# Kernel tuning notes

Measured on AMD Instinct MI355X. Metric: run time of the kernel, lower is better.

The kernel has to match this reference:

```python
import jax, jax.numpy as jnp
import numpy as np


def _lstm(x, w_ih, w_hh, b_ih, b_hh):
    # x: [B, T, D]; w_ih: [4H, D]; w_hh: [4H, H]. PyTorch gate order: i, f, g, o.
    B, T, D = x.shape
    H = w_hh.shape[1]
    # Precompute input contributions for all timesteps: [B, T, 4H]
    xg = jnp.einsum('btd,gd->btg', x, w_ih) + b_ih + b_hh
    xg = jnp.transpose(xg, (1, 0, 2))  # [T, B, 4H]

    def step(carry, xt):
        h, c = carry
        gates = xt + h @ w_hh.T  # [B, 4H]
        i, f, g, o = jnp.split(gates, 4, axis=-1)
        i = jax.nn.sigmoid(i)
        f = jax.nn.sigmoid(f)
        g = jnp.tanh(g)
        o = jax.nn.sigmoid(o)
        c = f * c + i * g
        h = o * jnp.tanh(c)
        return (h, c), h

    h0 = jnp.zeros((B, H), dtype=x.dtype)
    c0 = jnp.zeros((B, H), dtype=x.dtype)
    (_, _), hs = jax.lax.scan(step, (h0, c0), xg)
    return jnp.transpose(hs, (1, 0, 2))  # [B, T, H]


def setup_inputs() -> dict:
    key = jax.random.key(0)
    ks = jax.random.split(key, 11)
    B, T, D, H1, H2, OUT = 2048, 128, 128, 128, 64, 64
    s1 = 1.0 / np.sqrt(H1)
    s2 = 1.0 / np.sqrt(H2)
    return {
        'x': jax.random.normal(ks[0], (B, T, D), dtype=jnp.float32),
        'w_ih1': jax.random.uniform(ks[1], (4 * H1, D), jnp.float32, -s1, s1),
        'w_hh1': jax.random.uniform(ks[2], (4 * H1, H1), jnp.float32, -s1, s1),
        'b_ih1': jax.random.uniform(ks[3], (4 * H1,), jnp.float32, -s1, s1),
        'b_hh1': jax.random.uniform(ks[4], (4 * H1,), jnp.float32, -s1, s1),
        'w_ih2': jax.random.uniform(ks[5], (4 * H2, H1), jnp.float32, -s2, s2),
        'w_hh2': jax.random.uniform(ks[6], (4 * H2, H2), jnp.float32, -s2, s2),
        'b_ih2': jax.random.uniform(ks[7], (4 * H2,), jnp.float32, -s2, s2),
        'b_hh2': jax.random.uniform(ks[8], (4 * H2,), jnp.float32, -s2, s2),
        'w_dense': jax.random.uniform(ks[9], (OUT, H2), jnp.float32, -s2, s2),
        'b_dense': jax.random.uniform(ks[10], (OUT,), jnp.float32, -s2, s2),
    }


def reference(x, w_ih1, w_hh1, b_ih1, b_hh1, w_ih2, w_hh2, b_ih2, b_hh2, w_dense, b_dense):
    # Dropout is identity in eval mode.
    h = _lstm(x, w_ih1, w_hh1, b_ih1, b_hh1)          # [B, T, H1]
    h = _lstm(h, w_ih2, w_hh2, b_ih2, b_hh2)          # [B, T, H2]
    last = h[:, -1, :]                                 # [B, H2]
    return jax.nn.relu(last @ w_dense.T + b_dense)     # [B, 64]
```

## Files before the change

### kernel.cpp

```cpp
#include <hip/hip_runtime.h>
#include <hip/hip_bf16.h>

#define BB  2048
#define TT  128
#define DD  128
#define HH1 128
#define GG1 512
#define HH2 64
#define GG2 256
#define OO  64

typedef __attribute__((ext_vector_type(8))) short  short8;
typedef __attribute__((ext_vector_type(4))) float  floatx4;

#define PIN(x) asm volatile("" : "+v"(x))

#define OFF_WHH1 0
#define OFF_WIH1 131072
#define OFF_WIH2 262144
#define OFF_WHH2 327680
#define OFF_B1   360448
#define OFF_B2   362496
#define OFF_XBF  524288
#define OFF_H1S  67633152

__device__ __forceinline__ short f2bf(float f) {
  unsigned u = __float_as_uint(f);
  unsigned r = (u + 0x7FFFu + ((u >> 16) & 1u)) >> 16;
  return (short)r;
}
__device__ __forceinline__ float sigm(float x) {
  return __builtin_amdgcn_rcpf(1.0f + __expf(-x));
}
__device__ __forceinline__ float tanh_fast(float x) {
  return 1.0f - 2.0f * __builtin_amdgcn_rcpf(1.0f + __expf(2.0f * x));
}

__global__ void k_prep(const float* __restrict__ wih1, const float* __restrict__ whh1,
                       const float* __restrict__ bih1, const float* __restrict__ bhh1,
                       const float* __restrict__ wih2, const float* __restrict__ whh2,
                       const float* __restrict__ bih2, const float* __restrict__ bhh2,
                       char* __restrict__ ws) {
  short* WHH1 = (short*)(ws + OFF_WHH1);
  short* WIH1 = (short*)(ws + OFF_WIH1);
  short* WIH2 = (short*)(ws + OFF_WIH2);
  short* WHH2 = (short*)(ws + OFF_WHH2);
  float* B1 = (float*)(ws + OFF_B1);
  float* B2 = (float*)(ws + OFF_B2);
  int idx = blockIdx.x * blockDim.x + threadIdx.x;
  int stride = gridDim.x * blockDim.x;
  for (int i = idx; i < GG1 * DD; i += stride) { WIH1[i] = f2bf(wih1[i]); WHH1[i] = f2bf(whh1[i]); }
  for (int i = idx; i < GG2 * HH1; i += stride) WIH2[i] = f2bf(wih2[i]);
  for (int i = idx; i < GG2 * HH2; i += stride) WHH2[i] = f2bf(whh2[i]);
  for (int i = idx; i < GG1; i += stride) B1[i] = bih1[i] + bhh1[i];
  for (int i = idx; i < GG2; i += stride) B2[i] = bih2[i] + bhh2[i];
}

__global__ __launch_bounds__(256) void k_xcast(const float* __restrict__ x,
                                               short* __restrict__ xbf) {
  size_t i = ((size_t)blockIdx.x * 256 + threadIdx.x) * 8;
  float4 a = *(const float4*)&x[i];
  float4 b = *(const float4*)&x[i + 4];
  short8 o;
  o[0] = f2bf(a.x); o[1] = f2bf(a.y); o[2] = f2bf(a.z); o[3] = f2bf(a.w);
  o[4] = f2bf(b.x); o[5] = f2bf(b.y); o[6] = f2bf(b.z); o[7] = f2bf(b.w);
  *(short8*)&xbf[i] = o;
}

__global__ __launch_bounds__(512, 2) void k_rec1f(const char* __restrict__ ws,
                                                  short* __restrict__ h1s) {
  __shared__ short hbds[2][16 * 136];
  const short* WHH = (const short*)(ws + OFF_WHH1);
  const short* WIH = (const short*)(ws + OFF_WIH1);
  const short* XBF = (const short*)(ws + OFF_XBF);
  const float* B1 = (const float*)(ws + OFF_B1);
  const int lane = threadIdx.x & 63;
  const int wv = threadIdx.x >> 6;
  const int col = lane & 15, quad = lane >> 4;
  const int hc = wv * 16 + col;
  const int r0 = blockIdx.x * 8;

  short8 wh[4][4], wx[4][4];
#pragma unroll
  for (int gt = 0; gt < 4; ++gt)
#pragma unroll
    for (int kk = 0; kk < 4; ++kk) {
      wh[gt][kk] = *(const short8*)&WHH[(gt * 128 + hc) * HH1 + kk * 32 + quad * 8];
      wx[gt][kk] = *(const short8*)&WIH[(gt * 128 + hc) * DD + kk * 32 + quad * 8];
      PIN(wh[gt][kk]);
      PIN(wx[gt][kk]);
    }
  float bias[4];
#pragma unroll
  for (int gt = 0; gt < 4; ++gt) bias[gt] = B1[gt * 128 + hc];

  for (int i = threadIdx.x; i < 2 * 16 * 136; i += 512) ((short*)hbds)[i] = 0;

  const bool aload = (col < 8);
  const short* xbase = XBF + (size_t)(r0 + (col & 7)) * TT * DD;
  short8 ax_cur[4], ax_nxt[4];
#pragma unroll
  for (int kk = 0; kk < 4; ++kk) {
    short8 z = {0, 0, 0, 0, 0, 0, 0, 0};
    ax_cur[kk] = aload ? *(const short8*)&xbase[kk * 32 + quad * 8] : z;
    ax_nxt[kk] = z;
  }

  const int row0 = (quad & 1) * 4 + (quad >> 1) * 2;
  float c0 = 0.f, c1 = 0.f;
  __syncthreads();

  auto step = [&](int t, short* rbuf, short* wbuf) {
    if (t + 1 < TT && aload) {
#pragma unroll
      for (int kk = 0; kk < 4; ++kk)
        ax_nxt[kk] = *(const short8*)&xbase[(t + 1) * DD + kk * 32 + quad * 8];
    }
    floatx4 acc[4];
#pragma unroll
    for (int gt = 0; gt < 4; ++gt)
      acc[gt] = (floatx4){bias[gt], bias[gt], bias[gt], bias[gt]};
#pragma unroll
    for (int kk = 0; kk < 4; ++kk)
#pragma unroll
      for (int gt = 0; gt < 4; ++gt)
        acc[gt] = __builtin_amdgcn_mfma_f32_16x16x32_bf16(ax_cur[kk], wx[gt][kk], acc[gt], 0, 0, 0);
    short8 ah[4];
#pragma unroll
    for (int kk = 0; kk < 4; ++kk)
      ah[kk] = *(const short8*)&rbuf[col * 136 + kk * 32 + quad * 8];
#pragma unroll
    for (int kk = 0; kk < 4; ++kk)
#pragma unroll
      for (int gt = 0; gt < 4; ++gt)
        acc[gt] = __builtin_amdgcn_mfma_f32_16x16x32_bf16(ah[kk], wh[gt][kk], acc[gt], 0, 0, 0);

    float g0[4], g1[4];
#pragma unroll
    for (int gt = 0; gt < 4; ++gt) {
      float v2 = __shfl_xor(acc[gt][2], 32);
      float v3 = __shfl_xor(acc[gt][3], 32);
      g0[gt] = (quad < 2) ? acc[gt][0] : v2;
      g1[gt] = (quad < 2) ? acc[gt][1] : v3;
    }
    {
      float i0 = sigm(g0[0]), f0 = sigm(g0[1]), gg0 = tanh_fast(g0[2]), o0 = sigm(g0[3]);
      c0 = fmaf(f0, c0, i0 * gg0);
      float hA = o0 * tanh_fast(c0);
      float i1 = sigm(g1[0]), f1 = sigm(g1[1]), gg1 = tanh_fast(g1[2]), o1 = sigm(g1[3]);
      c1 = fmaf(f1, c1, i1 * gg1);
      float hB = o1 * tanh_fast(c1);
      short ha = f2bf(hA), hbv = f2bf(hB);
      wbuf[(row0)     * 136 + hc] = ha;
      wbuf[(row0 + 1) * 136 + hc] = hbv;
      h1s[((size_t)(r0 + row0)     * TT + t) * HH1 + hc] = ha;
      h1s[((size_t)(r0 + row0 + 1) * TT + t) * HH1 + hc] = hbv;
    }
    __syncthreads();
#pragma unroll
    for (int kk = 0; kk < 4; ++kk) ax_cur[kk] = ax_nxt[kk];
  };

  for (int t = 0; t < TT; t += 2) {
    step(t,     &hbds[0][0], &hbds[1][0]);
    step(t + 1, &hbds[1][0], &hbds[0][0]);
  }
}

__global__ __launch_bounds__(512, 2) void k_rec2f(const char* __restrict__ ws,
                                                  const short* __restrict__ h1s,
                                                  const float* __restrict__ wd,
                                                  const float* __restrict__ bd,
                                                  float* __restrict__ out) {
  __shared__ short hbuf[16 * 72];
  __shared__ float gsm[8 * 260];
  __shared__ float h2f[8 * HH2];
  const short* WHH = (const short*)(ws + OFF_WHH2);
  const short* WIH = (const short*)(ws + OFF_WIH2);
  const float* B2 = (const float*)(ws + OFF_B2);
  const int lane = threadIdx.x & 63;
  const int wv = threadIdx.x >> 6;
  const int col = lane & 15, quad = lane >> 4;
  const int n0 = wv * 32;
  const int r0 = blockIdx.x * 8;

  short8 wh[2][2], wx[2][4];
#pragma unroll
  for (int nt = 0; nt < 2; ++nt) {
#pragma unroll
    for (int kk = 0; kk < 2; ++kk) {
      wh[nt][kk] = *(const short8*)&WHH[(n0 + nt * 16 + col) * HH2 + kk * 32 + quad * 8];
      PIN(wh[nt][kk]);
    }
#pragma unroll
    for (int kk = 0; kk < 4; ++kk) {
      wx[nt][kk] = *(const short8*)&WIH[(n0 + nt * 16 + col) * HH1 + kk * 32 + quad * 8];
      PIN(wx[nt][kk]);
    }
  }
  float bias[2];
#pragma unroll
  for (int nt = 0; nt < 2; ++nt) bias[nt] = B2[n0 + nt * 16 + col];

  for (int i = threadIdx.x; i < 16 * 72; i += 512) hbuf[i] = 0;

  const bool aload = (col < 8);
  const short* h1base = h1s + (size_t)(r0 + (col & 7)) * TT * HH1;
  short8 ax_cur[4], ax_nxt[4];
#pragma unroll
  for (int kk = 0; kk < 4; ++kk) {
    short8 z = {0, 0, 0, 0, 0, 0, 0, 0};
    ax_cur[kk] = aload ? *(const short8*)&h1base[kk * 32 + quad * 8] : z;
    ax_nxt[kk] = z;
  }

  const int j = threadIdx.x & 63;
  const int rr = threadIdx.x >> 6;
  float cc = 0.f;
  __syncthreads();

  for (int t = 0; t < TT; ++t) {
    if (t + 1 < TT && aload) {
#pragma unroll
      for (int kk = 0; kk < 4; ++kk)
        ax_nxt[kk] = *(const short8*)&h1base[(t + 1) * HH1 + kk * 32 + quad * 8];
    }
    floatx4 acc[2];
#pragma unroll
    for (int nt = 0; nt < 2; ++nt)
      acc[nt] = (floatx4){bias[nt], bias[nt], bias[nt], bias[nt]};
#pragma unroll
    for (int kk = 0; kk < 4; ++kk)
#pragma unroll
      for (int nt = 0; nt < 2; ++nt)
        acc[nt] = __builtin_amdgcn_mfma_f32_16x16x32_bf16(ax_cur[kk], wx[nt][kk], acc[nt], 0, 0, 0);
    short8 ah[2];
#pragma unroll
    for (int kk = 0; kk < 2; ++kk)
      ah[kk] = *(const short8*)&hbuf[col * 72 + kk * 32 + quad * 8];
#pragma unroll
    for (int kk = 0; kk < 2; ++kk)
#pragma unroll
      for (int nt = 0; nt < 2; ++nt)
        acc[nt] = __builtin_amdgcn_mfma_f32_16x16x32_bf16(ah[kk], wh[nt][kk], acc[nt], 0, 0, 0);

    if (quad < 2) {
#pragma unroll
      for (int nt = 0; nt < 2; ++nt)
#pragma unroll
        for (int r = 0; r < 4; ++r)
          gsm[(quad * 4 + r) * 260 + n0 + nt * 16 + col] = acc[nt][r];
    }
    __syncthreads();

    {
      float i0 = gsm[rr * 260 + j],       f0 = gsm[rr * 260 + 64 + j];
      float g0 = gsm[rr * 260 + 128 + j], o0 = gsm[rr * 260 + 192 + j];
      cc = fmaf(sigm(f0), cc, sigm(i0) * tanh_fast(g0));
      float hh = sigm(o0) * tanh_fast(cc);
      hbuf[rr * 72 + j] = f2bf(hh);
      if (t == TT - 1) h2f[rr * HH2 + j] = hh;
    }
    __syncthreads();
#pragma unroll
    for (int kk = 0; kk < 4; ++kk) ax_cur[kk] = ax_nxt[kk];
  }

  {
    const int o = threadIdx.x & 63;
    const int r = threadIdx.x >> 6;
    float acc = bd[o];
    for (int k = 0; k < HH2; ++k)
      acc = fmaf(h2f[r * HH2 + k], wd[o * HH2 + k], acc);
    out[(size_t)(r0 + r) * OO + o] = fmaxf(acc, 0.f);
  }
}

extern "C" void kernel_launch(void* const* d_in, const int* in_sizes, int n_in,
                              void* d_out, int out_size, void* d_ws, size_t ws_size,
                              hipStream_t stream) {
  const float* x       = (const float*)d_in[0];
  const float* w_ih1   = (const float*)d_in[1];
  const float* w_hh1   = (const float*)d_in[2];
  const float* b_ih1   = (const float*)d_in[3];
  const float* b_hh1   = (const float*)d_in[4];
  const float* w_ih2   = (const float*)d_in[5];
  const float* w_hh2   = (const float*)d_in[6];
  const float* b_ih2   = (const float*)d_in[7];
  const float* b_hh2   = (const float*)d_in[8];
  const float* w_dense = (const float*)d_in[9];
  const float* b_dense = (const float*)d_in[10];
  char* ws = (char*)d_ws;
  short* xbf = (short*)(ws + OFF_XBF);
  short* h1s = (short*)(ws + OFF_H1S);
  float* out = (float*)d_out;

  hipLaunchKernelGGL(k_prep, dim3(256), dim3(256), 0, stream,
                     w_ih1, w_hh1, b_ih1, b_hh1, w_ih2, w_hh2, b_ih2, b_hh2, ws);
  hipLaunchKernelGGL(k_xcast, dim3((BB * TT * DD) / (256 * 8)), dim3(256), 0, stream, x, xbf);
  hipLaunchKernelGGL(k_rec1f, dim3(BB / 8), dim3(512), 0, stream, ws, h1s);
  hipLaunchKernelGGL(k_rec2f, dim3(BB / 8), dim3(512), 0, stream, ws, h1s, w_dense, b_dense, out);
}
```

Measured before the change: 443.5 us.

## Software-pipeline input projection one step ahead and use LDS-only barriers

```diff
diff --git a/kernel.cpp b/kernel.cpp
--- a/kernel.cpp
+++ b/kernel.cpp
@@ -34,6 +34,12 @@
 }
 __device__ __forceinline__ float tanh_fast(float x) {
   return 1.0f - 2.0f * __builtin_amdgcn_rcpf(1.0f + __expf(2.0f * x));
+}
+
+__device__ __forceinline__ void lds_barrier() {
+  asm volatile("s_waitcnt lgkmcnt(0)" ::: "memory");
+  __builtin_amdgcn_s_barrier();
+  asm volatile("" ::: "memory");
 }
 
 __global__ void k_prep(const float* __restrict__ wih1, const float* __restrict__ whh1,
@@ -98,50 +104,65 @@
 
   const bool aload = (col < 8);
   const short* xbase = XBF + (size_t)(r0 + (col & 7)) * TT * DD;
+  const short8 zz = {0, 0, 0, 0, 0, 0, 0, 0};
   short8 ax_cur[4], ax_nxt[4];
+
+  floatx4 accA[4], accB[4];
+  {
+    short8 ax0[4];
+#pragma unroll
+    for (int kk = 0; kk < 4; ++kk)
+      ax0[kk] = aload ? *(const short8*)&xbase[kk * 32 + quad * 8] : zz;
+#pragma unroll
+    for (int gt = 0; gt < 4; ++gt)
+      accA[gt] = (floatx4){bias[gt], bias[gt], bias[gt], bias[gt]};
+#pragma unroll
+    for (int kk = 0; kk < 4; ++kk)
+#pragma unroll
+      for (int gt = 0; gt < 4; ++gt)
+        accA[gt] = __builtin_amdgcn_mfma_f32_16x16x32_bf16(ax0[kk], wx[gt][kk], accA[gt], 0, 0, 0);
+  }
 #pragma unroll
   for (int kk = 0; kk < 4; ++kk) {
-    short8 z = {0, 0, 0, 0, 0, 0, 0, 0};
-    ax_cur[kk] = aload ? *(const short8*)&xbase[kk * 32 + quad * 8] : z;
-    ax_nxt[kk] = z;
+    ax_cur[kk] = aload ? *(const short8*)&xbase[DD + kk * 32 + quad * 8] : zz;
+    ax_nxt[kk] = ax_cur[kk];
   }
 
   const int row0 = (quad & 1) * 4 + (quad >> 1) * 2;
   float c0 = 0.f, c1 = 0.f;
   __syncthreads();
 
-  auto step = [&](int t, short* rbuf, short* wbuf) {
-    if (t + 1 < TT && aload) {
+  auto step = [&](int t, short* rbuf, short* wbuf, floatx4* A, floatx4* Bn) {
+    if (aload && t + 2 < TT) {
 #pragma unroll
       for (int kk = 0; kk < 4; ++kk)
-        ax_nxt[kk] = *(const short8*)&xbase[(t + 1) * DD + kk * 32 + quad * 8];
-    }
-    floatx4 acc[4];
+        ax_nxt[kk] = *(const short8*)&xbase[(t + 2) * DD + kk * 32 + quad * 8];
+    }
+    short8 ah[4];
+#pragma unroll
+    for (int kk = 0; kk < 4; ++kk)
+      ah[kk] = *(const short8*)&rbuf[col * 136 + kk * 32 + quad * 8];
+#pragma unroll
+    for (int kk = 0; kk < 4; ++kk)
+#pragma unroll
+      for (int gt = 0; gt < 4; ++gt)
+        A[gt] = __builtin_amdgcn_mfma_f32_16x16x32_bf16(ah[kk], wh[gt][kk], A[gt], 0, 0, 0);
 #pragma unroll
     for (int gt = 0; gt < 4; ++gt)
-      acc[gt] = (floatx4){bias[gt], bias[gt], bias[gt], bias[gt]};
+      Bn[gt] = (floatx4){bias[gt], bias[gt], bias[gt], bias[gt]};
 #pragma unroll
     for (int kk = 0; kk < 4; ++kk)
 #pragma unroll
       for (int gt = 0; gt < 4; ++gt)
-        acc[gt] = __builtin_amdgcn_mfma_f32_16x16x32_bf16(ax_cur[kk], wx[gt][kk], acc[gt], 0, 0, 0);
-    short8 ah[4];
-#pragma unroll
-    for (int kk = 0; kk < 4; ++kk)
-      ah[kk] = *(const short8*)&rbuf[col * 136 + kk * 32 + quad * 8];
-#pragma unroll
-    for (int kk = 0; kk < 4; ++kk)
-#pragma unroll
-      for (int gt = 0; gt < 4; ++gt)
-        acc[gt] = __builtin_amdgcn_mfma_f32_16x16x32_bf16(ah[kk], wh[gt][kk], acc[gt], 0, 0, 0);
+        Bn[gt] = __builtin_amdgcn_mfma_f32_16x16x32_bf16(ax_cur[kk], wx[gt][kk], Bn[gt], 0, 0, 0);
 
     float g0[4], g1[4];
 #pragma unroll
     for (int gt = 0; gt < 4; ++gt) {
-      float v2 = __shfl_xor(acc[gt][2], 32);
-      float v3 = __shfl_xor(acc[gt][3], 32);
-      g0[gt] = (quad < 2) ? acc[gt][0] : v2;
-      g1[gt] = (quad < 2) ? acc[gt][1] : v3;
+      float v2 = __shfl_xor(A[gt][2], 32);
+      float v3 = __shfl_xor(A[gt][3], 32);
+      g0[gt] = (quad < 2) ? A[gt][0] : v2;
+      g1[gt] = (quad < 2) ? A[gt][1] : v3;
     }
     {
       float i0 = sigm(g0[0]), f0 = sigm(g0[1]), gg0 = tanh_fast(g0[2]), o0 = sigm(g0[3]);
@@ -156,14 +177,14 @@
       h1s[((size_t)(r0 + row0)     * TT + t) * HH1 + hc] = ha;
       h1s[((size_t)(r0 + row0 + 1) * TT + t) * HH1 + hc] = hbv;
     }
-    __syncthreads();
+    lds_barrier();
 #pragma unroll
     for (int kk = 0; kk < 4; ++kk) ax_cur[kk] = ax_nxt[kk];
   };
 
   for (int t = 0; t < TT; t += 2) {
-    step(t,     &hbds[0][0], &hbds[1][0]);
-    step(t + 1, &hbds[1][0], &hbds[0][0]);
+    step(t,     &hbds[0][0], &hbds[1][0], accA, accB);
+    step(t + 1, &hbds[1][0], &hbds[0][0], accB, accA);
   }
 }
 
@@ -206,12 +227,28 @@
 
   const bool aload = (col < 8);
   const short* h1base = h1s + (size_t)(r0 + (col & 7)) * TT * HH1;
+  const short8 zz = {0, 0, 0, 0, 0, 0, 0, 0};
   short8 ax_cur[4], ax_nxt[4];
+
+  floatx4 accA[2], accB[2];
+  {
+    short8 ax0[4];
+#pragma unroll
+    for (int kk = 0; kk < 4; ++kk)
+      ax0[kk] = aload ? *(const short8*)&h1base[kk * 32 + quad * 8] : zz;
+#pragma unroll
+    for (int nt = 0; nt < 2; ++nt)
+      accA[nt] = (floatx4){bias[nt], bias[nt], bias[nt], bias[nt]};
+#pragma unroll
+    for (int kk = 0; kk < 4; ++kk)
+#pragma unroll
+      for (int nt = 0; nt < 2; ++nt)
+        accA[nt] = __builtin_amdgcn_mfma_f32_16x16x32_bf16(ax0[kk], wx[nt][kk], accA[nt], 0, 0, 0);
+  }
 #pragma unroll
   for (int kk = 0; kk < 4; ++kk) {
-    short8 z = {0, 0, 0, 0, 0, 0, 0, 0};
-    ax_cur[kk] = aload ? *(const short8*)&h1base[kk * 32 + quad * 8] : z;
-    ax_nxt[kk] = z;
+    ax_cur[kk] = aload ? *(const short8*)&h1base[HH1 + kk * 32 + quad * 8] : zz;
+    ax_nxt[kk] = ax_cur[kk];
   }
 
   const int j = threadIdx.x & 63;
@@ -219,21 +256,7 @@
   float cc = 0.f;
   __syncthreads();
 
-  for (int t = 0; t < TT; ++t) {
-    if (t + 1 < TT && aload) {
-#pragma unroll
-      for (int kk = 0; kk < 4; ++kk)
-        ax_nxt[kk] = *(const short8*)&h1base[(t + 1) * HH1 + kk * 32 + quad * 8];
-    }
-    floatx4 acc[2];
-#pragma unroll
-    for (int nt = 0; nt < 2; ++nt)
-      acc[nt] = (floatx4){bias[nt], bias[nt], bias[nt], bias[nt]};
-#pragma unroll
-    for (int kk = 0; kk < 4; ++kk)
-#pragma unroll
-      for (int nt = 0; nt < 2; ++nt)
-        acc[nt] = __builtin_amdgcn_mfma_f32_16x16x32_bf16(ax_cur[kk], wx[nt][kk], acc[nt], 0, 0, 0);
+  auto step = [&](int t, floatx4* A, floatx4* Bn) {
     short8 ah[2];
 #pragma unroll
     for (int kk = 0; kk < 2; ++kk)
@@ -242,16 +265,31 @@
     for (int kk = 0; kk < 2; ++kk)
 #pragma unroll
       for (int nt = 0; nt < 2; ++nt)
-        acc[nt] = __builtin_amdgcn_mfma_f32_16x16x32_bf16(ah[kk], wh[nt][kk], acc[nt], 0, 0, 0);
+        A[nt] = __builtin_amdgcn_mfma_f32_16x16x32_bf16(ah[kk], wh[nt][kk], A[nt], 0, 0, 0);
 
     if (quad < 2) {
 #pragma unroll
       for (int nt = 0; nt < 2; ++nt)
 #pragma unroll
         for (int r = 0; r < 4; ++r)
-          gsm[(quad * 4 + r) * 260 + n0 + nt * 16 + col] = acc[nt][r];
-    }
-    __syncthreads();
+          gsm[(quad * 4 + r) * 260 + n0 + nt * 16 + col] = A[nt][r];
+    }
+
+#pragma unroll
+    for (int nt = 0; nt < 2; ++nt)
+      Bn[nt] = (floatx4){bias[nt], bias[nt], bias[nt], bias[nt]};
+#pragma unroll
+    for (int kk = 0; kk < 4; ++kk)
+#pragma unroll
+      for (int nt = 0; nt < 2; ++nt)
+        Bn[nt] = __builtin_amdgcn_mfma_f32_16x16x32_bf16(ax_cur[kk], wx[nt][kk], Bn[nt], 0, 0, 0);
+    if (aload && t + 2 < TT) {
+#pragma unroll
+      for (int kk = 0; kk < 4; ++kk)
+        ax_nxt[kk] = *(const short8*)&h1base[(t + 2) * HH1 + kk * 32 + quad * 8];
+    }
+
+    lds_barrier();
 
     {
       float i0 = gsm[rr * 260 + j],       f0 = gsm[rr * 260 + 64 + j];
@@ -261,9 +299,14 @@
       hbuf[rr * 72 + j] = f2bf(hh);
       if (t == TT - 1) h2f[rr * HH2 + j] = hh;
     }
-    __syncthreads();
+    lds_barrier();
 #pragma unroll
     for (int kk = 0; kk < 4; ++kk) ax_cur[kk] = ax_nxt[kk];
+  };
+
+  for (int t = 0; t < TT; t += 2) {
+    step(t,     accA, accB);
+    step(t + 1, accB, accA);
   }
 
   {
```

Measured after the change: 424.6 us. 4.3% less time.
